# Kernel tuning notes

Hardware: AMD Instinct MI355X
Metric: run time of the kernel (lower is better)

Reference implementation:

```python
import jax, jax.numpy as jnp
import numpy as np

B, N, DIM = 2, 2048, 1024
HEADS, DIM_HEAD = 16, 64
ALIBI_HEADS = 8
NUM_MEM_KV = 4
SCALE = DIM_HEAD ** -0.5


def alibi_slopes(n):
    # standard ALiBi geometric slopes for power-of-2 head counts
    start = 2.0 ** (-8.0 / n)
    return jnp.array([start ** (k + 1) for k in range(n)], dtype=jnp.float32)


def alibi_bias(i, j, heads, total_heads):
    # symmetric ALiBi: bias = -|k_pos - q_pos| * slope; unbiased heads padded with zeros at front
    range_q = jnp.arange(j - i, j)          # query absolute positions (offset by mem kv)
    range_k = jnp.arange(j)
    rel = -jnp.abs(range_k[None, :] - range_q[:, None]).astype(jnp.float32)  # [i, j]
    slopes = alibi_slopes(heads)
    bias = slopes[:, None, None] * rel[None]                                  # [heads, i, j]
    pad = jnp.zeros((total_heads - heads, i, j), dtype=bias.dtype)
    return jnp.concatenate([pad, bias], axis=0)                               # [total_heads, i, j]


def setup_inputs() -> dict:
    key = jax.random.key(0)
    ks = jax.random.split(key, 7)
    w = lambda k, s: jax.random.normal(k, s, jnp.float32) * 0.02
    return {
        "x": jax.random.normal(ks[0], (B, N, DIM), jnp.float32),
        "mask": jnp.ones((B, N), dtype=bool),
        "Wq": w(ks[1], (DIM, HEADS * DIM_HEAD)),
        "Wk": w(ks[2], (DIM, HEADS * DIM_HEAD)),
        "Wv": w(ks[3], (DIM, HEADS * DIM_HEAD)),
        "Wo": w(ks[4], (HEADS * DIM_HEAD, DIM)),
        "mem_k": jax.random.normal(ks[5], (HEADS, NUM_MEM_KV, DIM_HEAD), jnp.float32),
        "mem_v": jax.random.normal(ks[6], (HEADS, NUM_MEM_KV, DIM_HEAD), jnp.float32),
    }


def reference(x, mask, Wq, Wk, Wv, Wo, mem_k, mem_v):
    b, n, _ = x.shape
    h, d, m = HEADS, DIM_HEAD, NUM_MEM_KV
    # QKV projections (Linear, no bias)
    q = (x @ Wq).reshape(b, n, h, d).transpose(0, 2, 1, 3)  # [b,h,n,d]
    k = (x @ Wk).reshape(b, n, h, d).transpose(0, 2, 1, 3)
    v = (x @ Wv).reshape(b, n, h, d).transpose(0, 2, 1, 3)
    # prepend learned memory key/values
    k = jnp.concatenate([jnp.broadcast_to(mem_k[None], (b, h, m, d)), k], axis=2)
    v = jnp.concatenate([jnp.broadcast_to(mem_v[None], (b, h, m, d)), v], axis=2)
    i, j = n, n + m
    # input mask padded with True over memory positions
    input_mask = jnp.concatenate([jnp.ones((b, m), dtype=bool), mask], axis=1)  # [b,j]
    # causal mask: key kj attendable by query qi iff kj - (j - i) <= qi (mem keys always visible)
    qpos = jnp.arange(i)[:, None]
    kpos = jnp.arange(j)[None, :]
    causal_allow = (kpos - (j - i)) <= qpos                                      # [i,j]
    allow = input_mask[:, None, None, :] & causal_allow[None, None]              # [b,1,i,j]
    bias = alibi_bias(i, j, ALIBI_HEADS, h)                                      # [h,i,j]
    scores = jnp.einsum('bhid,bhjd->bhij', q, k) * SCALE + bias[None]
    scores = jnp.where(allow, scores, jnp.finfo(scores.dtype).min)
    attn = jax.nn.softmax(scores, axis=-1)
    out = jnp.einsum('bhij,bhjd->bhid', attn, v)
    out = out.transpose(0, 2, 1, 3).reshape(b, n, h * d) @ Wo
    return out * mask[..., None].astype(out.dtype)
```

## Files before the change

kernel.cpp:

```cpp
#include <hip/hip_runtime.h>

typedef __bf16 bf16x8 __attribute__((ext_vector_type(8)));
typedef float f32x4 __attribute__((ext_vector_type(4)));
typedef unsigned short us8 __attribute__((ext_vector_type(8)));
typedef unsigned short ushort_t;
typedef unsigned int uint_t;

constexpr int BATCH = 2;
constexpr int SEQ   = 2048;
constexpr int DIM   = 1024;
constexpr int HEADS = 16;
constexpr int DH    = 64;
constexpr int NKV   = 4;
constexpr int KROWS = 2080;
constexpr int KVSTR = 133120;
constexpr float QSCALE = 0.18033688011112042f;

__device__ inline ushort_t f2bf(float f) {
  uint_t u = __builtin_bit_cast(uint_t, f);
  u += 0x7FFFu + ((u >> 16) & 1u);
  return (ushort_t)(u >> 16);
}

__device__ inline uint_t cvtpk(float a, float b) {
  uint_t r;
  asm("v_cvt_pk_bf16_f32 %0, %1, %2" : "=v"(r) : "v"(a), "v"(b));
  return r;
}

__device__ inline float ex2(float x) { return __builtin_amdgcn_exp2f(x); }

__device__ inline bf16x8 mk8(uint_t a, uint_t b, uint_t c, uint_t d) {
  union { uint_t u[4]; bf16x8 v; } x;
  x.u[0] = a; x.u[1] = b; x.u[2] = c; x.u[3] = d;
  return x.v;
}

__device__ inline size_t swz(int row, int k) {
  return ((size_t)(row >> 7) << 17) +
         (size_t)(((k >> 3) << 7) + (row & 127)) * 8 + (k & 7);
}

__device__ inline int koff(int j, int d) {
  return ((j >> 4) << 10) + ((d >> 3) << 7) + ((j & 15) << 3) + (d & 7);
}
__device__ inline int voff(int j, int d) {
  int w = j & 31;
  int kap = ((w & 12) << 1) | (w & 3) | ((w >> 4) << 2);
  return ((j >> 5) << 11) + ((kap >> 3) << 9) + (d << 3) + (kap & 7);
}

__device__ inline void g2l16(const ushort_t* g, ushort_t* l) {
  __builtin_amdgcn_global_load_lds(
      (const __attribute__((address_space(1))) void*)g,
      (__attribute__((address_space(3))) void*)l, 16, 0, 0);
}

__global__ __launch_bounds__(256) void prep_kernel(
    const float* __restrict__ x,
    const float* __restrict__ W0, const float* __restrict__ W1,
    const float* __restrict__ W2, const float* __restrict__ W3,
    const float* __restrict__ memk, const float* __restrict__ memv,
    ushort_t* __restrict__ xb,
    ushort_t* __restrict__ T0, ushort_t* __restrict__ T1,
    ushort_t* __restrict__ T2, ushort_t* __restrict__ T3,
    ushort_t* __restrict__ Vt, ushort_t* __restrict__ Ka)
{
  __shared__ float tile[32][33];
  int bid = blockIdx.x, t = threadIdx.x;
  if (bid < 2048) {
    int idx = bid * 256 + t;
    const float4* s = (const float4*)x;
    float4 a = s[idx * 2], bq = s[idx * 2 + 1];
    us8 o;
    o[0] = f2bf(a.x);  o[1] = f2bf(a.y);  o[2] = f2bf(a.z);  o[3] = f2bf(a.w);
    o[4] = f2bf(bq.x); o[5] = f2bf(bq.y); o[6] = f2bf(bq.z); o[7] = f2bf(bq.w);
    int e = idx * 8, row = e >> 10, k = e & 1023;
    *(us8*)&xb[swz(row, k)] = o;
  } else if (bid < 6144) {
    int tb = bid - 2048, z = tb >> 10, r2 = tb & 1023;
    int bx = r2 & 31, by = r2 >> 5;
    const float* W = (z == 0) ? W0 : (z == 1) ? W1 : (z == 2) ? W2 : W3;
    ushort_t* T = (z == 0) ? T0 : (z == 1) ? T1 : (z == 2) ? T2 : T3;
    float sc = (z == 0) ? QSCALE : 1.0f;
    int tx = t & 31, ty = t >> 5;
    int kb = bx * 32, nb = by * 32;
    for (int y = ty; y < 32; y += 8)
      tile[y][tx] = W[(size_t)(kb + y) * 1024 + nb + tx];
    __syncthreads();
    for (int y = ty; y < 32; y += 8)
      T[swz(nb + y, kb + tx)] = f2bf(tile[tx][y] * sc);
  } else {
    int idx = (bid - 6144) * 256 + t;
    if (idx < 8192) {
      int j = idx & 3, d = (idx >> 2) & 63, h = (idx >> 8) & 15, b = idx >> 12;
      Vt[(size_t)(b * 16 + h) * KVSTR + voff(j, d)] =
          f2bf(memv[((size_t)h * NKV + j) * DH + d]);
    } else if (idx < 16384) {
      int k2 = idx - 8192;
      int d = k2 & 63, j = (k2 >> 6) & 3, h = (k2 >> 8) & 15, b = k2 >> 12;
      Ka[(size_t)(b * 16 + h) * KVSTR + koff(j, d)] =
          f2bf(memk[((size_t)h * NKV + j) * DH + d]);
    }
  }
}

__global__ __launch_bounds__(256, 6) void gemm_bt(
    const ushort_t* __restrict__ A,
    const ushort_t* __restrict__ Wt0, const ushort_t* __restrict__ Wt1,
    const ushort_t* __restrict__ Wt2,
    ushort_t* __restrict__ C0, ushort_t* __restrict__ Ka,
    ushort_t* __restrict__ Vt)
{
  __shared__ ushort_t As[8192];
  __shared__ ushort_t Bs[4096];
  int bid = blockIdx.x;
  int xcd = bid & 7, g = bid >> 3;
  int z = g >> 6, rem = g & 63;
  int my = (xcd >> 1) * 8 + (rem >> 3);
  int nx = (xcd & 1) * 8 + (rem & 7);
  const ushort_t* Wt = (z == 1) ? Wt1 : (z == 2) ? Wt2 : Wt0;
  int t = threadIdx.x;
  int lane = t & 63, wave = t >> 6;
  int col = lane & 15, quad = lane >> 4;
  int m0 = my * 128, n0 = nx * 64;
  int moff = wave * 32;
  int nhalf = nx & 1;

  const ushort_t* Abase = A  + ((size_t)(m0 >> 7) << 17);
  const ushort_t* Bbase = Wt + ((size_t)(nx >> 1) << 17);
  int so = wave * 2048 + lane * 8;

  f32x4 acc[2][4] = {};

  for (int k0 = 0; k0 < DIM; k0 += 64) {
    __syncthreads();
    const ushort_t* Ak = Abase + ((size_t)k0 << 7);
    const ushort_t* Bk = Bbase + ((size_t)k0 << 7);
#pragma unroll
    for (int c2 = 0; c2 < 4; c2++)
      g2l16(Ak + so + c2 * 512, &As[so + c2 * 512]);
#pragma unroll
    for (int c2 = 0; c2 < 2; c2++) {
      int ko = wave * 2 + c2;
      g2l16(Bk + ko * 1024 + nhalf * 512 + lane * 8, &Bs[ko * 512 + lane * 8]);
    }
    __syncthreads();
#pragma unroll
    for (int kc = 0; kc < 2; kc++) {
      bf16x8 af[2], bfr[4];
#pragma unroll
      for (int mi = 0; mi < 2; mi++)
        af[mi] = *(const bf16x8*)&As[(kc * 4 + quad) * 1024 + (moff + mi * 16 + col) * 8];
#pragma unroll
      for (int ni = 0; ni < 4; ni++)
        bfr[ni] = *(const bf16x8*)&Bs[(kc * 4 + quad) * 512 + (ni * 16 + col) * 8];
#pragma unroll
      for (int mi = 0; mi < 2; mi++)
#pragma unroll
        for (int ni = 0; ni < 4; ni++)
          acc[mi][ni] = __builtin_amdgcn_mfma_f32_16x16x32_bf16(
              af[mi], bfr[ni], acc[mi][ni], 0, 0, 0);
    }
  }

  if (z == 0) {
#pragma unroll
    for (int mi = 0; mi < 2; mi++) {
      int row0 = m0 + moff + mi * 16 + quad * 4;
#pragma unroll
      for (int ni = 0; ni < 4; ni++) {
        int cn = n0 + ni * 16 + col;
#pragma unroll
        for (int r = 0; r < 4; r++)
          C0[swz(row0 + r, cn)] = f2bf(acc[mi][ni][r]);
      }
    }
  } else if (z == 1) {
#pragma unroll
    for (int mi = 0; mi < 2; mi++) {
      int gi = m0 + moff + mi * 16 + quad * 4;
      int bq = gi >> 11, i = gi & 2047;
#pragma unroll
      for (int ni = 0; ni < 4; ni++) {
        int feat = n0 + ni * 16 + col;
        int hh = feat >> 6, dd = feat & 63;
        size_t base = (size_t)(bq * 16 + hh) * KVSTR;
#pragma unroll
        for (int r = 0; r < 4; r++)
          Ka[base + koff(i + r + NKV, dd)] = f2bf(acc[mi][ni][r]);
      }
    }
  } else {
#pragma unroll
    for (int mi = 0; mi < 2; mi++) {
      int gi = m0 + moff + mi * 16 + quad * 4;
      int bq = gi >> 11, i = gi & 2047;
#pragma unroll
      for (int ni = 0; ni < 4; ni++) {
        int feat = n0 + ni * 16 + col;
        int hh = feat >> 6, dd = feat & 63;
        size_t vb = (size_t)(bq * 16 + hh) * KVSTR;
#pragma unroll
        for (int r = 0; r < 4; r++)
          Vt[vb + voff(i + r + NKV, dd)] = f2bf(acc[mi][ni][r]);
      }
    }
  }
}

__global__ __launch_bounds__(256, 4) void gemm_out64(
    const ushort_t* __restrict__ A, const ushort_t* __restrict__ Wt,
    float* __restrict__ Cf)
{
  __shared__ ushort_t As[4096];
  __shared__ ushort_t Bs[4096];
  int bid = blockIdx.x;
  int xcd = bid & 7, g = bid >> 3;
  int my = xcd * 8 + (g >> 4);
  int nx = g & 15;
  int t = threadIdx.x;
  int lane = t & 63, wave = t >> 6;
  int col = lane & 15, quad = lane >> 4;
  int m0 = my * 64, n0 = nx * 64;
  int mhalf = my & 1;
  int nhalf = nx & 1;

  const ushort_t* Abase = A  + ((size_t)(my >> 1) << 17);
  const ushort_t* Bbase = Wt + ((size_t)(nx >> 1) << 17);

  f32x4 acc[4] = {};

  for (int k0 = 0; k0 < DIM; k0 += 64) {
    __syncthreads();
    const ushort_t* Ak = Abase + ((size_t)k0 << 7);
    const ushort_t* Bk = Bbase + ((size_t)k0 << 7);
#pragma unroll
    for (int c2 = 0; c2 < 2; c2++) {
      int ko = wave * 2 + c2;
      g2l16(Ak + ko * 1024 + mhalf * 512 + lane * 8, &As[ko * 512 + lane * 8]);
      g2l16(Bk + ko * 1024 + nhalf * 512 + lane * 8, &Bs[ko * 512 + lane * 8]);
    }
    __syncthreads();
#pragma unroll
    for (int kc = 0; kc < 2; kc++) {
      bf16x8 af, bfr[4];
      af = *(const bf16x8*)&As[(kc * 4 + quad) * 512 + (wave * 16 + col) * 8];
#pragma unroll
      for (int ni = 0; ni < 4; ni++)
        bfr[ni] = *(const bf16x8*)&Bs[(kc * 4 + quad) * 512 + (ni * 16 + col) * 8];
#pragma unroll
      for (int ni = 0; ni < 4; ni++)
        acc[ni] = __builtin_amdgcn_mfma_f32_16x16x32_bf16(
            af, bfr[ni], acc[ni], 0, 0, 0);
    }
  }

  int row0 = m0 + wave * 16 + quad * 4;
#pragma unroll
  for (int ni = 0; ni < 4; ni++) {
    int cn = n0 + ni * 16 + col;
#pragma unroll
    for (int r = 0; r < 4; r++)
      Cf[(size_t)(row0 + r) * DIM + cn] = acc[ni][r];
  }
}

#define STRIPC(jbX, I0, Q00, Q01, Q10, Q11,                                   \
               O0A, O1A, O2A, O3A, OLA, O0B, O1B, O2B, O3B, OLB,              \
               K0, K1, K2, K3, V0, V1, V2, V3)                                \
  {                                                                           \
    f32x4 s0a = {}, s1a = {}, s0b = {}, s1b = {};                             \
    __builtin_amdgcn_s_setprio(1);                                            \
    s0a = __builtin_amdgcn_mfma_f32_16x16x32_bf16(K0, Q00, s0a, 0, 0, 0);     \
    s0a = __builtin_amdgcn_mfma_f32_16x16x32_bf16(K1, Q01, s0a, 0, 0, 0);     \
    s1a = __builtin_amdgcn_mfma_f32_16x16x32_bf16(K2, Q00, s1a, 0, 0, 0);     \
    s1a = __builtin_amdgcn_mfma_f32_16x16x32_bf16(K3, Q01, s1a, 0, 0, 0);     \
    s0b = __builtin_amdgcn_mfma_f32_16x16x32_bf16(K0, Q10, s0b, 0, 0, 0);     \
    s0b = __builtin_amdgcn_mfma_f32_16x16x32_bf16(K1, Q11, s0b, 0, 0, 0);     \
    s1b = __builtin_amdgcn_mfma_f32_16x16x32_bf16(K2, Q10, s1b, 0, 0, 0);     \
    s1b = __builtin_amdgcn_mfma_f32_16x16x32_bf16(K3, Q11, s1b, 0, 0, 0);     \
    __builtin_amdgcn_s_setprio(0);                                            \
    float fD0 = (float)((jbX) + quad * 4 - (I0) - col - NKV);                 \
    bf16x8 pa, pb;                                                            \
    {                                                                         \
      f32x4 e0, e1;                                                           \
      if ((jbX) <= (I0) - 27) {                                               \
        _Pragma("unroll")                                                     \
        for (int r = 0; r < 4; r++) {                                         \
          e0[r] = ex2(fmaf(slope2, fD0 + (float)r, s0a[r]));                  \
          e1[r] = ex2(fmaf(slope2, fD0 + 16.0f + (float)r, s1a[r]));          \
        }                                                                     \
      } else {                                                                \
        _Pragma("unroll")                                                     \
        for (int r = 0; r < 4; r++) {                                         \
          float f0 = fD0 + (float)r, f1 = fD0 + 16.0f + (float)r;             \
          float w0 = fmaf(slope2, f0, s0a[r]);                                \
          float w1 = fmaf(slope2, f1, s1a[r]);                                \
          w0 = (f0 <= 0.0f) ? w0 : -1e30f;                                    \
          w1 = (f1 <= 0.0f) ? w1 : -1e30f;                                    \
          e0[r] = ex2(w0); e1[r] = ex2(w1);                                   \
        }                                                                     \
      }                                                                       \
      pa = mk8(cvtpk(e0[0], e0[1]), cvtpk(e0[2], e0[3]),                      \
               cvtpk(e1[0], e1[1]), cvtpk(e1[2], e1[3]));                     \
    }                                                                         \
    {                                                                         \
      float fDb = fD0 - 16.0f;                                                \
      f32x4 e0, e1;                                                           \
      if ((jbX) <= (I0) - 11) {                                               \
        _Pragma("unroll")                                                     \
        for (int r = 0; r < 4; r++) {                                         \
          e0[r] = ex2(fmaf(slope2, fDb + (float)r, s0b[r]));                  \
          e1[r] = ex2(fmaf(slope2, fDb + 16.0f + (float)r, s1b[r]));          \
        }                                                                     \
      } else {                                                                \
        _Pragma("unroll")                                                     \
        for (int r = 0; r < 4; r++) {                                         \
          float f0 = fDb + (float)r, f1 = fDb + 16.0f + (float)r;             \
          float w0 = fmaf(slope2, f0, s0b[r]);                                \
          float w1 = fmaf(slope2, f1, s1b[r]);                                \
          w0 = (f0 <= 0.0f) ? w0 : -1e30f;                                    \
          w1 = (f1 <= 0.0f) ? w1 : -1e30f;                                    \
          e0[r] = ex2(w0); e1[r] = ex2(w1);                                   \
        }                                                                     \
      }                                                                       \
      pb = mk8(cvtpk(e0[0], e0[1]), cvtpk(e0[2], e0[3]),                      \
               cvtpk(e1[0], e1[1]), cvtpk(e1[2], e1[3]));                     \
    }                                                                         \
    __builtin_amdgcn_s_setprio(1);                                            \
    O0A = __builtin_amdgcn_mfma_f32_16x16x32_bf16(pa, V0, O0A, 0, 0, 0);      \
    O1A = __builtin_amdgcn_mfma_f32_16x16x32_bf16(pa, V1, O1A, 0, 0, 0);      \
    O2A = __builtin_amdgcn_mfma_f32_16x16x32_bf16(pa, V2, O2A, 0, 0, 0);      \
    O3A = __builtin_amdgcn_mfma_f32_16x16x32_bf16(pa, V3, O3A, 0, 0, 0);      \
    OLA = __builtin_amdgcn_mfma_f32_16x16x32_bf16(pa, ones, OLA, 0, 0, 0);    \
    O0B = __builtin_amdgcn_mfma_f32_16x16x32_bf16(pb, V0, O0B, 0, 0, 0);      \
    O1B = __builtin_amdgcn_mfma_f32_16x16x32_bf16(pb, V1, O1B, 0, 0, 0);      \
    O2B = __builtin_amdgcn_mfma_f32_16x16x32_bf16(pb, V2, O2B, 0, 0, 0);      \
    O3B = __builtin_amdgcn_mfma_f32_16x16x32_bf16(pb, V3, O3B, 0, 0, 0);      \
    OLB = __builtin_amdgcn_mfma_f32_16x16x32_bf16(pb, ones, OLB, 0, 0, 0);    \
    __builtin_amdgcn_s_setprio(0);                                            \
  }

#define SUBITER(jbX, jpref, K0, K1, K2, K3, V0, V1, V2, V3)                   \
  {                                                                           \
    STRIPC(jbX, i0y, qy00, qy01, qy10, qy11,                                  \
           yo0a, yo1a, yo2a, yo3a, yla, yo0b, yo1b, yo2b, yo3b, ylb,          \
           K0, K1, K2, K3, V0, V1, V2, V3);                                   \
    if ((jbX) < jendx) {                                                      \
      STRIPC(jbX, i0x, qx00, qx01, qx10, qx11,                                \
             xo0a, xo1a, xo2a, xo3a, xla, xo0b, xo1b, xo2b, xo3b, xlb,        \
             K0, K1, K2, K3, V0, V1, V2, V3);                                 \
    }                                                                         \
    int jc = (jpref) > 2048 ? 2048 : (jpref);                                 \
    int aK = jc * 64 + kOff;                                                  \
    K0 = *(const bf16x8*)&Kbh[aK];                                            \
    K1 = *(const bf16x8*)&Kbh[aK + 512];                                      \
    K2 = *(const bf16x8*)&Kbh[aK + 1024];                                     \
    K3 = *(const bf16x8*)&Kbh[aK + 1536];                                     \
    int aV = jc * 64 + vOff;                                                  \
    V0 = *(const bf16x8*)&Vbh[aV];                                            \
    V1 = *(const bf16x8*)&Vbh[aV + 128];                                      \
    V2 = *(const bf16x8*)&Vbh[aV + 256];                                      \
    V3 = *(const bf16x8*)&Vbh[aV + 384];                                      \
  }

__global__ __launch_bounds__(256) void attn_kernel(
    const ushort_t* __restrict__ Q, const ushort_t* __restrict__ Ka,
    const ushort_t* __restrict__ Vt, ushort_t* __restrict__ AO)
{
  __shared__ __align__(16) float Cmb[2][10][64][4];
  int t = threadIdx.x, lane = t & 63, wave = t >> 6;
  int col = lane & 15, quad = lane >> 4;
  int bid = blockIdx.x;
  int xcd = bid & 7, slot = bid >> 3;
  int bh = xcd + 8 * (slot >> 4);
  int b = bh >> 4, h = bh & 15;
  int u = slot & 15;
  int pi = u * 2 + (wave >> 1);
  int h2 = wave & 1;
  int p2 = wave >> 1;
  float slope2 = (h < 8) ? 0.0f : exp2f(-(float)(h - 7)) * 1.4426950408889634f;

  const ushort_t* Kbh = Ka + (size_t)bh * KVSTR;
  const ushort_t* Vbh = Vt + (size_t)bh * KVSTR;

  us8 ones_u = {0x3F80, 0x3F80, 0x3F80, 0x3F80, 0x3F80, 0x3F80, 0x3F80, 0x3F80};
  bf16x8 ones = __builtin_bit_cast(bf16x8, ones_u);

  int kOff = quad * 128 + col * 8;
  int vOff = quad * 512 + col * 8;

  int i0x = pi * 32;
  int i0y = 2016 - pi * 32;
  int jendx = ((i0x + 67) >> 5) << 5;
  int jendy = ((i0y + 67) >> 5) << 5;

  bf16x8 qx00 = *(const bf16x8*)&Q[swz(b * SEQ + i0x + col, h * DH + quad * 8)];
  bf16x8 qx01 = *(const bf16x8*)&Q[swz(b * SEQ + i0x + col, h * DH + 32 + quad * 8)];
  bf16x8 qx10 = *(const bf16x8*)&Q[swz(b * SEQ + i0x + 16 + col, h * DH + quad * 8)];
  bf16x8 qx11 = *(const bf16x8*)&Q[swz(b * SEQ + i0x + 16 + col, h * DH + 32 + quad * 8)];
  bf16x8 qy00 = *(const bf16x8*)&Q[swz(b * SEQ + i0y + col, h * DH + quad * 8)];
  bf16x8 qy01 = *(const bf16x8*)&Q[swz(b * SEQ + i0y + col, h * DH + 32 + quad * 8)];
  bf16x8 qy10 = *(const bf16x8*)&Q[swz(b * SEQ + i0y + 16 + col, h * DH + quad * 8)];
  bf16x8 qy11 = *(const bf16x8*)&Q[swz(b * SEQ + i0y + 16 + col, h * DH + 32 + quad * 8)];

  f32x4 xo0a = {}, xo1a = {}, xo2a = {}, xo3a = {}, xla = {};
  f32x4 xo0b = {}, xo1b = {}, xo2b = {}, xo3b = {}, xlb = {};
  f32x4 yo0a = {}, yo1a = {}, yo2a = {}, yo3a = {}, yla = {};
  f32x4 yo0b = {}, yo1b = {}, yo2b = {}, yo3b = {}, ylb = {};

  bf16x8 ka0, ka1, ka2, ka3, va0, va1, va2, va3;
  bf16x8 kb0, kb1, kb2, kb3, vb0, vb1, vb2, vb3;
  int jb0 = h2 * 32;
  {
    int aK = jb0 * 64 + kOff, aV = jb0 * 64 + vOff;
    ka0 = *(const bf16x8*)&Kbh[aK];
    ka1 = *(const bf16x8*)&Kbh[aK + 512];
    ka2 = *(const bf16x8*)&Kbh[aK + 1024];
    ka3 = *(const bf16x8*)&Kbh[aK + 1536];
    va0 = *(const bf16x8*)&Vbh[aV];
    va1 = *(const bf16x8*)&Vbh[aV + 128];
    va2 = *(const bf16x8*)&Vbh[aV + 256];
    va3 = *(const bf16x8*)&Vbh[aV + 384];
    int j1 = jb0 + 64;
    int bK = j1 * 64 + kOff, bV = j1 * 64 + vOff;
    kb0 = *(const bf16x8*)&Kbh[bK];
    kb1 = *(const bf16x8*)&Kbh[bK + 512];
    kb2 = *(const bf16x8*)&Kbh[bK + 1024];
    kb3 = *(const bf16x8*)&Kbh[bK + 1536];
    vb0 = *(const bf16x8*)&Vbh[bV];
    vb1 = *(const bf16x8*)&Vbh[bV + 128];
    vb2 = *(const bf16x8*)&Vbh[bV + 256];
    vb3 = *(const bf16x8*)&Vbh[bV + 384];
  }

  int ntrip = (jendy - jb0 + 127) >> 7;
  int jb = jb0;
#pragma unroll 1
  for (int tr = 0; tr < ntrip; tr++, jb += 128) {
    SUBITER(jb, jb + 128, ka0, ka1, ka2, ka3, va0, va1, va2, va3);
    SUBITER(jb + 64, jb + 192, kb0, kb1, kb2, kb3, vb0, vb1, vb2, vb3);
  }

  if (h2 == 1) {
    *(f32x4*)&Cmb[p2][0][lane][0] = yo0a;
    *(f32x4*)&Cmb[p2][1][lane][0] = yo1a;
    *(f32x4*)&Cmb[p2][2][lane][0] = yo2a;
    *(f32x4*)&Cmb[p2][3][lane][0] = yo3a;
    *(f32x4*)&Cmb[p2][4][lane][0] = yla;
    *(f32x4*)&Cmb[p2][5][lane][0] = yo0b;
    *(f32x4*)&Cmb[p2][6][lane][0] = yo1b;
    *(f32x4*)&Cmb[p2][7][lane][0] = yo2b;
    *(f32x4*)&Cmb[p2][8][lane][0] = yo3b;
    *(f32x4*)&Cmb[p2][9][lane][0] = ylb;
  }
  __syncthreads();
  if (h2 == 0) {
    yo0a += *(const f32x4*)&Cmb[p2][0][lane][0];
    yo1a += *(const f32x4*)&Cmb[p2][1][lane][0];
    yo2a += *(const f32x4*)&Cmb[p2][2][lane][0];
    yo3a += *(const f32x4*)&Cmb[p2][3][lane][0];
    yla  += *(const f32x4*)&Cmb[p2][4][lane][0];
    yo0b += *(const f32x4*)&Cmb[p2][5][lane][0];
    yo1b += *(const f32x4*)&Cmb[p2][6][lane][0];
    yo2b += *(const f32x4*)&Cmb[p2][7][lane][0];
    yo3b += *(const f32x4*)&Cmb[p2][8][lane][0];
    ylb  += *(const f32x4*)&Cmb[p2][9][lane][0];
#pragma unroll
    for (int r = 0; r < 4; r++) {
      float linv = __builtin_amdgcn_rcpf(yla[r]);
      int row = b * SEQ + i0y + quad * 4 + r;
      AO[swz(row, h * DH + col)]      = f2bf(yo0a[r] * linv);
      AO[swz(row, h * DH + 16 + col)] = f2bf(yo1a[r] * linv);
      AO[swz(row, h * DH + 32 + col)] = f2bf(yo2a[r] * linv);
      AO[swz(row, h * DH + 48 + col)] = f2bf(yo3a[r] * linv);
    }
#pragma unroll
    for (int r = 0; r < 4; r++) {
      float linv = __builtin_amdgcn_rcpf(ylb[r]);
      int row = b * SEQ + i0y + 16 + quad * 4 + r;
      AO[swz(row, h * DH + col)]      = f2bf(yo0b[r] * linv);
      AO[swz(row, h * DH + 16 + col)] = f2bf(yo1b[r] * linv);
      AO[swz(row, h * DH + 32 + col)] = f2bf(yo2b[r] * linv);
      AO[swz(row, h * DH + 48 + col)] = f2bf(yo3b[r] * linv);
    }
  }
  __syncthreads();

  if (h2 == 1) {
    *(f32x4*)&Cmb[p2][0][lane][0] = xo0a;
    *(f32x4*)&Cmb[p2][1][lane][0] = xo1a;
    *(f32x4*)&Cmb[p2][2][lane][0] = xo2a;
    *(f32x4*)&Cmb[p2][3][lane][0] = xo3a;
    *(f32x4*)&Cmb[p2][4][lane][0] = xla;
    *(f32x4*)&Cmb[p2][5][lane][0] = xo0b;
    *(f32x4*)&Cmb[p2][6][lane][0] = xo1b;
    *(f32x4*)&Cmb[p2][7][lane][0] = xo2b;
    *(f32x4*)&Cmb[p2][8][lane][0] = xo3b;
    *(f32x4*)&Cmb[p2][9][lane][0] = xlb;
  }
  __syncthreads();
  if (h2 == 0) {
    xo0a += *(const f32x4*)&Cmb[p2][0][lane][0];
    xo1a += *(const f32x4*)&Cmb[p2][1][lane][0];
    xo2a += *(const f32x4*)&Cmb[p2][2][lane][0];
    xo3a += *(const f32x4*)&Cmb[p2][3][lane][0];
    xla  += *(const f32x4*)&Cmb[p2][4][lane][0];
    xo0b += *(const f32x4*)&Cmb[p2][5][lane][0];
    xo1b += *(const f32x4*)&Cmb[p2][6][lane][0];
    xo2b += *(const f32x4*)&Cmb[p2][7][lane][0];
    xo3b += *(const f32x4*)&Cmb[p2][8][lane][0];
    xlb  += *(const f32x4*)&Cmb[p2][9][lane][0];
#pragma unroll
    for (int r = 0; r < 4; r++) {
      float linv = __builtin_amdgcn_rcpf(xla[r]);
      int row = b * SEQ + i0x + quad * 4 + r;
      AO[swz(row, h * DH + col)]      = f2bf(xo0a[r] * linv);
      AO[swz(row, h * DH + 16 + col)] = f2bf(xo1a[r] * linv);
      AO[swz(row, h * DH + 32 + col)] = f2bf(xo2a[r] * linv);
      AO[swz(row, h * DH + 48 + col)] = f2bf(xo3a[r] * linv);
    }
#pragma unroll
    for (int r = 0; r < 4; r++) {
      float linv = __builtin_amdgcn_rcpf(xlb[r]);
      int row = b * SEQ + i0x + 16 + quad * 4 + r;
      AO[swz(row, h * DH + col)]      = f2bf(xo0b[r] * linv);
      AO[swz(row, h * DH + 16 + col)] = f2bf(xo1b[r] * linv);
      AO[swz(row, h * DH + 32 + col)] = f2bf(xo2b[r] * linv);
      AO[swz(row, h * DH + 48 + col)] = f2bf(xo3b[r] * linv);
    }
  }
}
#undef SUBITER
#undef STRIPC

extern "C" void kernel_launch(void* const* d_in, const int* in_sizes, int n_in,
                              void* d_out, int out_size, void* d_ws, size_t ws_size,
                              hipStream_t stream)
{
  const float* x    = (const float*)d_in[0];
  const float* Wq   = (const float*)d_in[2];
  const float* Wk   = (const float*)d_in[3];
  const float* Wv   = (const float*)d_in[4];
  const float* Wo   = (const float*)d_in[5];
  const float* memk = (const float*)d_in[6];
  const float* memv = (const float*)d_in[7];
  float* out = (float*)d_out;

  char* ws = (char*)d_ws;
  size_t off = 0;
  auto alloc = [&](size_t bytes) {
    char* p = ws + off;
    off += (bytes + 255) & ~(size_t)255;
    return p;
  };
  ushort_t* WqT = (ushort_t*)alloc((size_t)1024 * 1024 * 2);
  ushort_t* WkT = (ushort_t*)alloc((size_t)1024 * 1024 * 2);
  ushort_t* WvT = (ushort_t*)alloc((size_t)1024 * 1024 * 2);
  ushort_t* WoT = (ushort_t*)alloc((size_t)1024 * 1024 * 2);
  ushort_t* xb  = (ushort_t*)alloc((size_t)4096 * 1024 * 2);
  ushort_t* Qb  = (ushort_t*)alloc((size_t)4096 * 1024 * 2);
  ushort_t* Ka  = (ushort_t*)alloc((size_t)32 * KVSTR * 2);
  ushort_t* Vt  = (ushort_t*)alloc((size_t)32 * KVSTR * 2);
  ushort_t* AO  = xb;

  prep_kernel<<<dim3(6208), dim3(256), 0, stream>>>(
      x, Wq, Wk, Wv, Wo, memk, memv, xb, WqT, WkT, WvT, WoT, Vt, Ka);
  gemm_bt<<<dim3(1536), dim3(256), 0, stream>>>(xb, WqT, WkT, WvT, Qb, Ka, Vt);
  attn_kernel<<<dim3(512), dim3(256), 0, stream>>>(Qb, Ka, Vt, AO);
  gemm_out64<<<dim3(1024), dim3(256), 0, stream>>>(AO, WoT, out);
}
```

Before: 188.5 us.

## Fuse QKV GEMM blocks to share A tiles; split attention keys across four waves

The QKV projection now uses one 512-thread block per output tile. Each block computes Q, K and V together, so each loaded x tile is reused for three weight tiles instead of being fetched by three separate blocks. The attention kernel now has each block process two query-strip pairs in sequence, with all four waves splitting the key range in stride-256 chunks, and the partial results of three waves are merged by wave 0. This cuts redundant activation loads and changes how work is balanced across waves. In exchange it adds more LDS traffic and barriers per strip, and gives the GEMM fewer, larger blocks.

```diff
diff --git a/kernel.cpp b/kernel.cpp
--- a/kernel.cpp
+++ b/kernel.cpp
@@ -105,7 +105,7 @@
   }
 }
 
-__global__ __launch_bounds__(256, 6) void gemm_bt(
+__global__ __launch_bounds__(512) void gemm_bt(
     const ushort_t* __restrict__ A,
     const ushort_t* __restrict__ Wt0, const ushort_t* __restrict__ Wt1,
     const ushort_t* __restrict__ Wt2,
@@ -113,98 +113,87 @@
     ushort_t* __restrict__ Vt)
 {
   __shared__ ushort_t As[8192];
-  __shared__ ushort_t Bs[4096];
+  __shared__ ushort_t Bs[12288];
   int bid = blockIdx.x;
   int xcd = bid & 7, g = bid >> 3;
-  int z = g >> 6, rem = g & 63;
-  int my = (xcd >> 1) * 8 + (rem >> 3);
-  int nx = (xcd & 1) * 8 + (rem & 7);
-  const ushort_t* Wt = (z == 1) ? Wt1 : (z == 2) ? Wt2 : Wt0;
+  int my = (xcd >> 1) * 8 + (g >> 3);
+  int nx = (xcd & 1) * 8 + (g & 7);
   int t = threadIdx.x;
   int lane = t & 63, wave = t >> 6;
   int col = lane & 15, quad = lane >> 4;
   int m0 = my * 128, n0 = nx * 64;
-  int moff = wave * 32;
+  int moff = wave * 16;
   int nhalf = nx & 1;
 
-  const ushort_t* Abase = A  + ((size_t)(m0 >> 7) << 17);
-  const ushort_t* Bbase = Wt + ((size_t)(nx >> 1) << 17);
-  int so = wave * 2048 + lane * 8;
-
-  f32x4 acc[2][4] = {};
+  const ushort_t* Abase = A + ((size_t)(m0 >> 7) << 17);
+  size_t boff = (size_t)(nx >> 1) << 17;
+  const ushort_t* Bb0 = Wt0 + boff;
+  const ushort_t* Bb1 = Wt1 + boff;
+  const ushort_t* Bb2 = Wt2 + boff;
+  int t8 = t * 8;
+  int bo = (t >> 6) * 1024 + nhalf * 512 + (t & 63) * 8;
+
+  f32x4 acc[3][4] = {};
 
   for (int k0 = 0; k0 < DIM; k0 += 64) {
     __syncthreads();
     const ushort_t* Ak = Abase + ((size_t)k0 << 7);
-    const ushort_t* Bk = Bbase + ((size_t)k0 << 7);
-#pragma unroll
-    for (int c2 = 0; c2 < 4; c2++)
-      g2l16(Ak + so + c2 * 512, &As[so + c2 * 512]);
-#pragma unroll
-    for (int c2 = 0; c2 < 2; c2++) {
-      int ko = wave * 2 + c2;
-      g2l16(Bk + ko * 1024 + nhalf * 512 + lane * 8, &Bs[ko * 512 + lane * 8]);
-    }
+    size_t ko2 = (size_t)k0 << 7;
+    g2l16(Ak + t8, &As[t8]);
+    g2l16(Ak + t8 + 4096, &As[t8 + 4096]);
+    g2l16(Bb0 + ko2 + bo, &Bs[t8]);
+    g2l16(Bb1 + ko2 + bo, &Bs[4096 + t8]);
+    g2l16(Bb2 + ko2 + bo, &Bs[8192 + t8]);
     __syncthreads();
 #pragma unroll
     for (int kc = 0; kc < 2; kc++) {
-      bf16x8 af[2], bfr[4];
-#pragma unroll
-      for (int mi = 0; mi < 2; mi++)
-        af[mi] = *(const bf16x8*)&As[(kc * 4 + quad) * 1024 + (moff + mi * 16 + col) * 8];
-#pragma unroll
-      for (int ni = 0; ni < 4; ni++)
-        bfr[ni] = *(const bf16x8*)&Bs[(kc * 4 + quad) * 512 + (ni * 16 + col) * 8];
-#pragma unroll
-      for (int mi = 0; mi < 2; mi++)
+      bf16x8 af = *(const bf16x8*)&As[(kc * 4 + quad) * 1024 + (moff + col) * 8];
+#pragma unroll
+      for (int z = 0; z < 3; z++) {
+        bf16x8 bfr[4];
 #pragma unroll
         for (int ni = 0; ni < 4; ni++)
-          acc[mi][ni] = __builtin_amdgcn_mfma_f32_16x16x32_bf16(
-              af[mi], bfr[ni], acc[mi][ni], 0, 0, 0);
-    }
-  }
-
-  if (z == 0) {
-#pragma unroll
-    for (int mi = 0; mi < 2; mi++) {
-      int row0 = m0 + moff + mi * 16 + quad * 4;
-#pragma unroll
-      for (int ni = 0; ni < 4; ni++) {
-        int cn = n0 + ni * 16 + col;
-#pragma unroll
-        for (int r = 0; r < 4; r++)
-          C0[swz(row0 + r, cn)] = f2bf(acc[mi][ni][r]);
-      }
-    }
-  } else if (z == 1) {
-#pragma unroll
-    for (int mi = 0; mi < 2; mi++) {
-      int gi = m0 + moff + mi * 16 + quad * 4;
-      int bq = gi >> 11, i = gi & 2047;
-#pragma unroll
-      for (int ni = 0; ni < 4; ni++) {
-        int feat = n0 + ni * 16 + col;
-        int hh = feat >> 6, dd = feat & 63;
-        size_t base = (size_t)(bq * 16 + hh) * KVSTR;
-#pragma unroll
-        for (int r = 0; r < 4; r++)
-          Ka[base + koff(i + r + NKV, dd)] = f2bf(acc[mi][ni][r]);
-      }
-    }
-  } else {
-#pragma unroll
-    for (int mi = 0; mi < 2; mi++) {
-      int gi = m0 + moff + mi * 16 + quad * 4;
-      int bq = gi >> 11, i = gi & 2047;
-#pragma unroll
-      for (int ni = 0; ni < 4; ni++) {
-        int feat = n0 + ni * 16 + col;
-        int hh = feat >> 6, dd = feat & 63;
-        size_t vb = (size_t)(bq * 16 + hh) * KVSTR;
-#pragma unroll
-        for (int r = 0; r < 4; r++)
-          Vt[vb + voff(i + r + NKV, dd)] = f2bf(acc[mi][ni][r]);
-      }
+          bfr[ni] = *(const bf16x8*)&Bs[z * 4096 + (kc * 4 + quad) * 512 + (ni * 16 + col) * 8];
+#pragma unroll
+        for (int ni = 0; ni < 4; ni++)
+          acc[z][ni] = __builtin_amdgcn_mfma_f32_16x16x32_bf16(
+              af, bfr[ni], acc[z][ni], 0, 0, 0);
+      }
+    }
+  }
+
+  int row0 = m0 + moff + quad * 4;
+  {
+#pragma unroll
+    for (int ni = 0; ni < 4; ni++) {
+      int cn = n0 + ni * 16 + col;
+#pragma unroll
+      for (int r = 0; r < 4; r++)
+        C0[swz(row0 + r, cn)] = f2bf(acc[0][ni][r]);
+    }
+  }
+  {
+    int bq = row0 >> 11, i = row0 & 2047;
+#pragma unroll
+    for (int ni = 0; ni < 4; ni++) {
+      int feat = n0 + ni * 16 + col;
+      int hh = feat >> 6, dd = feat & 63;
+      size_t base = (size_t)(bq * 16 + hh) * KVSTR;
+#pragma unroll
+      for (int r = 0; r < 4; r++)
+        Ka[base + koff(i + r + NKV, dd)] = f2bf(acc[1][ni][r]);
+    }
+  }
+  {
+    int bq = row0 >> 11, i = row0 & 2047;
+#pragma unroll
+    for (int ni = 0; ni < 4; ni++) {
+      int feat = n0 + ni * 16 + col;
+      int hh = feat >> 6, dd = feat & 63;
+      size_t vb = (size_t)(bq * 16 + hh) * KVSTR;
+#pragma unroll
+      for (int r = 0; r < 4; r++)
+        Vt[vb + voff(i + r + NKV, dd)] = f2bf(acc[2][ni][r]);
     }
   }
 }
@@ -369,17 +358,14 @@
     const ushort_t* __restrict__ Q, const ushort_t* __restrict__ Ka,
     const ushort_t* __restrict__ Vt, ushort_t* __restrict__ AO)
 {
-  __shared__ __align__(16) float Cmb[2][10][64][4];
+  __shared__ __align__(16) float Cmb[3][10][64][4];
   int t = threadIdx.x, lane = t & 63, wave = t >> 6;
   int col = lane & 15, quad = lane >> 4;
   int bid = blockIdx.x;
   int xcd = bid & 7, slot = bid >> 3;
   int bh = xcd + 8 * (slot >> 4);
   int b = bh >> 4, h = bh & 15;
-  int u = slot & 15;
-  int pi = u * 2 + (wave >> 1);
-  int h2 = wave & 1;
-  int p2 = wave >> 1;
+  int q = slot & 15;
   float slope2 = (h < 8) ? 0.0f : exp2f(-(float)(h - 7)) * 1.4426950408889634f;
 
   const ushort_t* Kbh = Ka + (size_t)bh * KVSTR;
@@ -391,145 +377,157 @@
   int kOff = quad * 128 + col * 8;
   int vOff = quad * 512 + col * 8;
 
-  int i0x = pi * 32;
-  int i0y = 2016 - pi * 32;
-  int jendx = ((i0x + 67) >> 5) << 5;
-  int jendy = ((i0y + 67) >> 5) << 5;
-
-  bf16x8 qx00 = *(const bf16x8*)&Q[swz(b * SEQ + i0x + col, h * DH + quad * 8)];
-  bf16x8 qx01 = *(const bf16x8*)&Q[swz(b * SEQ + i0x + col, h * DH + 32 + quad * 8)];
-  bf16x8 qx10 = *(const bf16x8*)&Q[swz(b * SEQ + i0x + 16 + col, h * DH + quad * 8)];
-  bf16x8 qx11 = *(const bf16x8*)&Q[swz(b * SEQ + i0x + 16 + col, h * DH + 32 + quad * 8)];
-  bf16x8 qy00 = *(const bf16x8*)&Q[swz(b * SEQ + i0y + col, h * DH + quad * 8)];
-  bf16x8 qy01 = *(const bf16x8*)&Q[swz(b * SEQ + i0y + col, h * DH + 32 + quad * 8)];
-  bf16x8 qy10 = *(const bf16x8*)&Q[swz(b * SEQ + i0y + 16 + col, h * DH + quad * 8)];
-  bf16x8 qy11 = *(const bf16x8*)&Q[swz(b * SEQ + i0y + 16 + col, h * DH + 32 + quad * 8)];
-
-  f32x4 xo0a = {}, xo1a = {}, xo2a = {}, xo3a = {}, xla = {};
-  f32x4 xo0b = {}, xo1b = {}, xo2b = {}, xo3b = {}, xlb = {};
-  f32x4 yo0a = {}, yo1a = {}, yo2a = {}, yo3a = {}, yla = {};
-  f32x4 yo0b = {}, yo1b = {}, yo2b = {}, yo3b = {}, ylb = {};
-
-  bf16x8 ka0, ka1, ka2, ka3, va0, va1, va2, va3;
-  bf16x8 kb0, kb1, kb2, kb3, vb0, vb1, vb2, vb3;
-  int jb0 = h2 * 32;
-  {
-    int aK = jb0 * 64 + kOff, aV = jb0 * 64 + vOff;
-    ka0 = *(const bf16x8*)&Kbh[aK];
-    ka1 = *(const bf16x8*)&Kbh[aK + 512];
-    ka2 = *(const bf16x8*)&Kbh[aK + 1024];
-    ka3 = *(const bf16x8*)&Kbh[aK + 1536];
-    va0 = *(const bf16x8*)&Vbh[aV];
-    va1 = *(const bf16x8*)&Vbh[aV + 128];
-    va2 = *(const bf16x8*)&Vbh[aV + 256];
-    va3 = *(const bf16x8*)&Vbh[aV + 384];
-    int j1 = jb0 + 64;
-    int bK = j1 * 64 + kOff, bV = j1 * 64 + vOff;
-    kb0 = *(const bf16x8*)&Kbh[bK];
-    kb1 = *(const bf16x8*)&Kbh[bK + 512];
-    kb2 = *(const bf16x8*)&Kbh[bK + 1024];
-    kb3 = *(const bf16x8*)&Kbh[bK + 1536];
-    vb0 = *(const bf16x8*)&Vbh[bV];
-    vb1 = *(const bf16x8*)&Vbh[bV + 128];
-    vb2 = *(const bf16x8*)&Vbh[bV + 256];
-    vb3 = *(const bf16x8*)&Vbh[bV + 384];
-  }
-
-  int ntrip = (jendy - jb0 + 127) >> 7;
-  int jb = jb0;
+  for (int pr = 0; pr < 2; pr++) {
+    int m = pr ? (31 - q) : q;
+    int i0x = m * 32;
+    int i0y = 2016 - m * 32;
+    int jendx = ((i0x + 67) >> 5) << 5;
+    int jendy = ((i0y + 67) >> 5) << 5;
+
+    bf16x8 qx00 = *(const bf16x8*)&Q[swz(b * SEQ + i0x + col, h * DH + quad * 8)];
+    bf16x8 qx01 = *(const bf16x8*)&Q[swz(b * SEQ + i0x + col, h * DH + 32 + quad * 8)];
+    bf16x8 qx10 = *(const bf16x8*)&Q[swz(b * SEQ + i0x + 16 + col, h * DH + quad * 8)];
+    bf16x8 qx11 = *(const bf16x8*)&Q[swz(b * SEQ + i0x + 16 + col, h * DH + 32 + quad * 8)];
+    bf16x8 qy00 = *(const bf16x8*)&Q[swz(b * SEQ + i0y + col, h * DH + quad * 8)];
+    bf16x8 qy01 = *(const bf16x8*)&Q[swz(b * SEQ + i0y + col, h * DH + 32 + quad * 8)];
+    bf16x8 qy10 = *(const bf16x8*)&Q[swz(b * SEQ + i0y + 16 + col, h * DH + quad * 8)];
+    bf16x8 qy11 = *(const bf16x8*)&Q[swz(b * SEQ + i0y + 16 + col, h * DH + 32 + quad * 8)];
+
+    f32x4 xo0a = {}, xo1a = {}, xo2a = {}, xo3a = {}, xla = {};
+    f32x4 xo0b = {}, xo1b = {}, xo2b = {}, xo3b = {}, xlb = {};
+    f32x4 yo0a = {}, yo1a = {}, yo2a = {}, yo3a = {}, yla = {};
+    f32x4 yo0b = {}, yo1b = {}, yo2b = {}, yo3b = {}, ylb = {};
+
+    bf16x8 ka0, ka1, ka2, ka3, va0, va1, va2, va3;
+    bf16x8 kb0, kb1, kb2, kb3, vb0, vb1, vb2, vb3;
+    int jb0 = wave * 32;
+    {
+      int aK = jb0 * 64 + kOff, aV = jb0 * 64 + vOff;
+      ka0 = *(const bf16x8*)&Kbh[aK];
+      ka1 = *(const bf16x8*)&Kbh[aK + 512];
+      ka2 = *(const bf16x8*)&Kbh[aK + 1024];
+      ka3 = *(const bf16x8*)&Kbh[aK + 1536];
+      va0 = *(const bf16x8*)&Vbh[aV];
+      va1 = *(const bf16x8*)&Vbh[aV + 128];
+      va2 = *(const bf16x8*)&Vbh[aV + 256];
+      va3 = *(const bf16x8*)&Vbh[aV + 384];
+      int j1 = jb0 + 128;
+      int bK = j1 * 64 + kOff, bV = j1 * 64 + vOff;
+      kb0 = *(const bf16x8*)&Kbh[bK];
+      kb1 = *(const bf16x8*)&Kbh[bK + 512];
+      kb2 = *(const bf16x8*)&Kbh[bK + 1024];
+      kb3 = *(const bf16x8*)&Kbh[bK + 1536];
+      vb0 = *(const bf16x8*)&Vbh[bV];
+      vb1 = *(const bf16x8*)&Vbh[bV + 128];
+      vb2 = *(const bf16x8*)&Vbh[bV + 256];
+      vb3 = *(const bf16x8*)&Vbh[bV + 384];
+    }
+
+    int ntrip = (jendy - jb0 + 255) >> 8;
+    int jb = jb0;
 #pragma unroll 1
-  for (int tr = 0; tr < ntrip; tr++, jb += 128) {
-    SUBITER(jb, jb + 128, ka0, ka1, ka2, ka3, va0, va1, va2, va3);
-    SUBITER(jb + 64, jb + 192, kb0, kb1, kb2, kb3, vb0, vb1, vb2, vb3);
-  }
-
-  if (h2 == 1) {
-    *(f32x4*)&Cmb[p2][0][lane][0] = yo0a;
-    *(f32x4*)&Cmb[p2][1][lane][0] = yo1a;
-    *(f32x4*)&Cmb[p2][2][lane][0] = yo2a;
-    *(f32x4*)&Cmb[p2][3][lane][0] = yo3a;
-    *(f32x4*)&Cmb[p2][4][lane][0] = yla;
-    *(f32x4*)&Cmb[p2][5][lane][0] = yo0b;
-    *(f32x4*)&Cmb[p2][6][lane][0] = yo1b;
-    *(f32x4*)&Cmb[p2][7][lane][0] = yo2b;
-    *(f32x4*)&Cmb[p2][8][lane][0] = yo3b;
-    *(f32x4*)&Cmb[p2][9][lane][0] = ylb;
-  }
-  __syncthreads();
-  if (h2 == 0) {
-    yo0a += *(const f32x4*)&Cmb[p2][0][lane][0];
-    yo1a += *(const f32x4*)&Cmb[p2][1][lane][0];
-    yo2a += *(const f32x4*)&Cmb[p2][2][lane][0];
-    yo3a += *(const f32x4*)&Cmb[p2][3][lane][0];
-    yla  += *(const f32x4*)&Cmb[p2][4][lane][0];
-    yo0b += *(const f32x4*)&Cmb[p2][5][lane][0];
-    yo1b += *(const f32x4*)&Cmb[p2][6][lane][0];
-    yo2b += *(const f32x4*)&Cmb[p2][7][lane][0];
-    yo3b += *(const f32x4*)&Cmb[p2][8][lane][0];
-    ylb  += *(const f32x4*)&Cmb[p2][9][lane][0];
-#pragma unroll
-    for (int r = 0; r < 4; r++) {
-      float linv = __builtin_amdgcn_rcpf(yla[r]);
-      int row = b * SEQ + i0y + quad * 4 + r;
-      AO[swz(row, h * DH + col)]      = f2bf(yo0a[r] * linv);
-      AO[swz(row, h * DH + 16 + col)] = f2bf(yo1a[r] * linv);
-      AO[swz(row, h * DH + 32 + col)] = f2bf(yo2a[r] * linv);
-      AO[swz(row, h * DH + 48 + col)] = f2bf(yo3a[r] * linv);
-    }
-#pragma unroll
-    for (int r = 0; r < 4; r++) {
-      float linv = __builtin_amdgcn_rcpf(ylb[r]);
-      int row = b * SEQ + i0y + 16 + quad * 4 + r;
-      AO[swz(row, h * DH + col)]      = f2bf(yo0b[r] * linv);
-      AO[swz(row, h * DH + 16 + col)] = f2bf(yo1b[r] * linv);
-      AO[swz(row, h * DH + 32 + col)] = f2bf(yo2b[r] * linv);
-      AO[swz(row, h * DH + 48 + col)] = f2bf(yo3b[r] * linv);
-    }
-  }
-  __syncthreads();
-
-  if (h2 == 1) {
-    *(f32x4*)&Cmb[p2][0][lane][0] = xo0a;
-    *(f32x4*)&Cmb[p2][1][lane][0] = xo1a;
-    *(f32x4*)&Cmb[p2][2][lane][0] = xo2a;
-    *(f32x4*)&Cmb[p2][3][lane][0] = xo3a;
-    *(f32x4*)&Cmb[p2][4][lane][0] = xla;
-    *(f32x4*)&Cmb[p2][5][lane][0] = xo0b;
-    *(f32x4*)&Cmb[p2][6][lane][0] = xo1b;
-    *(f32x4*)&Cmb[p2][7][lane][0] = xo2b;
-    *(f32x4*)&Cmb[p2][8][lane][0] = xo3b;
-    *(f32x4*)&Cmb[p2][9][lane][0] = xlb;
-  }
-  __syncthreads();
-  if (h2 == 0) {
-    xo0a += *(const f32x4*)&Cmb[p2][0][lane][0];
-    xo1a += *(const f32x4*)&Cmb[p2][1][lane][0];
-    xo2a += *(const f32x4*)&Cmb[p2][2][lane][0];
-    xo3a += *(const f32x4*)&Cmb[p2][3][lane][0];
-    xla  += *(const f32x4*)&Cmb[p2][4][lane][0];
-    xo0b += *(const f32x4*)&Cmb[p2][5][lane][0];
-    xo1b += *(const f32x4*)&Cmb[p2][6][lane][0];
-    xo2b += *(const f32x4*)&Cmb[p2][7][lane][0];
-    xo3b += *(const f32x4*)&Cmb[p2][8][lane][0];
-    xlb  += *(const f32x4*)&Cmb[p2][9][lane][0];
-#pragma unroll
-    for (int r = 0; r < 4; r++) {
-      float linv = __builtin_amdgcn_rcpf(xla[r]);
-      int row = b * SEQ + i0x + quad * 4 + r;
-      AO[swz(row, h * DH + col)]      = f2bf(xo0a[r] * linv);
-      AO[swz(row, h * DH + 16 + col)] = f2bf(xo1a[r] * linv);
-      AO[swz(row, h * DH + 32 + col)] = f2bf(xo2a[r] * linv);
-      AO[swz(row, h * DH + 48 + col)] = f2bf(xo3a[r] * linv);
-    }
-#pragma unroll
-    for (int r = 0; r < 4; r++) {
-      float linv = __builtin_amdgcn_rcpf(xlb[r]);
-      int row = b * SEQ + i0x + 16 + quad * 4 + r;
-      AO[swz(row, h * DH + col)]      = f2bf(xo0b[r] * linv);
-      AO[swz(row, h * DH + 16 + col)] = f2bf(xo1b[r] * linv);
-      AO[swz(row, h * DH + 32 + col)] = f2bf(xo2b[r] * linv);
-      AO[swz(row, h * DH + 48 + col)] = f2bf(xo3b[r] * linv);
-    }
+    for (int tr = 0; tr < ntrip; tr++, jb += 256) {
+      SUBITER(jb, jb + 256, ka0, ka1, ka2, ka3, va0, va1, va2, va3);
+      SUBITER(jb + 128, jb + 384, kb0, kb1, kb2, kb3, vb0, vb1, vb2, vb3);
+    }
+
+    if (wave) {
+      int w = wave - 1;
+      *(f32x4*)&Cmb[w][0][lane][0] = yo0a;
+      *(f32x4*)&Cmb[w][1][lane][0] = yo1a;
+      *(f32x4*)&Cmb[w][2][lane][0] = yo2a;
+      *(f32x4*)&Cmb[w][3][lane][0] = yo3a;
+      *(f32x4*)&Cmb[w][4][lane][0] = yla;
+      *(f32x4*)&Cmb[w][5][lane][0] = yo0b;
+      *(f32x4*)&Cmb[w][6][lane][0] = yo1b;
+      *(f32x4*)&Cmb[w][7][lane][0] = yo2b;
+      *(f32x4*)&Cmb[w][8][lane][0] = yo3b;
+      *(f32x4*)&Cmb[w][9][lane][0] = ylb;
+    }
+    __syncthreads();
+    if (wave == 0) {
+#pragma unroll
+      for (int w = 0; w < 3; w++) {
+        yo0a += *(const f32x4*)&Cmb[w][0][lane][0];
+        yo1a += *(const f32x4*)&Cmb[w][1][lane][0];
+        yo2a += *(const f32x4*)&Cmb[w][2][lane][0];
+        yo3a += *(const f32x4*)&Cmb[w][3][lane][0];
+        yla  += *(const f32x4*)&Cmb[w][4][lane][0];
+        yo0b += *(const f32x4*)&Cmb[w][5][lane][0];
+        yo1b += *(const f32x4*)&Cmb[w][6][lane][0];
+        yo2b += *(const f32x4*)&Cmb[w][7][lane][0];
+        yo3b += *(const f32x4*)&Cmb[w][8][lane][0];
+        ylb  += *(const f32x4*)&Cmb[w][9][lane][0];
+      }
+#pragma unroll
+      for (int r = 0; r < 4; r++) {
+        float linv = __builtin_amdgcn_rcpf(yla[r]);
+        int row = b * SEQ + i0y + quad * 4 + r;
+        AO[swz(row, h * DH + col)]      = f2bf(yo0a[r] * linv);
+        AO[swz(row, h * DH + 16 + col)] = f2bf(yo1a[r] * linv);
+        AO[swz(row, h * DH + 32 + col)] = f2bf(yo2a[r] * linv);
+        AO[swz(row, h * DH + 48 + col)] = f2bf(yo3a[r] * linv);
+      }
+#pragma unroll
+      for (int r = 0; r < 4; r++) {
+        float linv = __builtin_amdgcn_rcpf(ylb[r]);
+        int row = b * SEQ + i0y + 16 + quad * 4 + r;
+        AO[swz(row, h * DH + col)]      = f2bf(yo0b[r] * linv);
+        AO[swz(row, h * DH + 16 + col)] = f2bf(yo1b[r] * linv);
+        AO[swz(row, h * DH + 32 + col)] = f2bf(yo2b[r] * linv);
+        AO[swz(row, h * DH + 48 + col)] = f2bf(yo3b[r] * linv);
+      }
+    }
+    __syncthreads();
+
+    if (wave) {
+      int w = wave - 1;
+      *(f32x4*)&Cmb[w][0][lane][0] = xo0a;
+      *(f32x4*)&Cmb[w][1][lane][0] = xo1a;
+      *(f32x4*)&Cmb[w][2][lane][0] = xo2a;
+      *(f32x4*)&Cmb[w][3][lane][0] = xo3a;
+      *(f32x4*)&Cmb[w][4][lane][0] = xla;
+      *(f32x4*)&Cmb[w][5][lane][0] = xo0b;
+      *(f32x4*)&Cmb[w][6][lane][0] = xo1b;
+      *(f32x4*)&Cmb[w][7][lane][0] = xo2b;
+      *(f32x4*)&Cmb[w][8][lane][0] = xo3b;
+      *(f32x4*)&Cmb[w][9][lane][0] = xlb;
+    }
+    __syncthreads();
+    if (wave == 0) {
+#pragma unroll
+      for (int w = 0; w < 3; w++) {
+        xo0a += *(const f32x4*)&Cmb[w][0][lane][0];
+        xo1a += *(const f32x4*)&Cmb[w][1][lane][0];
+        xo2a += *(const f32x4*)&Cmb[w][2][lane][0];
+        xo3a += *(const f32x4*)&Cmb[w][3][lane][0];
+        xla  += *(const f32x4*)&Cmb[w][4][lane][0];
+        xo0b += *(const f32x4*)&Cmb[w][5][lane][0];
+        xo1b += *(const f32x4*)&Cmb[w][6][lane][0];
+        xo2b += *(const f32x4*)&Cmb[w][7][lane][0];
+        xo3b += *(const f32x4*)&Cmb[w][8][lane][0];
+        xlb  += *(const f32x4*)&Cmb[w][9][lane][0];
+      }
+#pragma unroll
+      for (int r = 0; r < 4; r++) {
+        float linv = __builtin_amdgcn_rcpf(xla[r]);
+        int row = b * SEQ + i0x + quad * 4 + r;
+        AO[swz(row, h * DH + col)]      = f2bf(xo0a[r] * linv);
+        AO[swz(row, h * DH + 16 + col)] = f2bf(xo1a[r] * linv);
+        AO[swz(row, h * DH + 32 + col)] = f2bf(xo2a[r] * linv);
+        AO[swz(row, h * DH + 48 + col)] = f2bf(xo3a[r] * linv);
+      }
+#pragma unroll
+      for (int r = 0; r < 4; r++) {
+        float linv = __builtin_amdgcn_rcpf(xlb[r]);
+        int row = b * SEQ + i0x + 16 + quad * 4 + r;
+        AO[swz(row, h * DH + col)]      = f2bf(xo0b[r] * linv);
+        AO[swz(row, h * DH + 16 + col)] = f2bf(xo1b[r] * linv);
+        AO[swz(row, h * DH + 32 + col)] = f2bf(xo2b[r] * linv);
+        AO[swz(row, h * DH + 48 + col)] = f2bf(xo3b[r] * linv);
+      }
+    }
+    __syncthreads();
   }
 }
 #undef SUBITER
@@ -567,7 +565,7 @@
 
   prep_kernel<<<dim3(6208), dim3(256), 0, stream>>>(
       x, Wq, Wk, Wv, Wo, memk, memv, xb, WqT, WkT, WvT, WoT, Vt, Ka);
-  gemm_bt<<<dim3(1536), dim3(256), 0, stream>>>(xb, WqT, WkT, WvT, Qb, Ka, Vt);
+  gemm_bt<<<dim3(512), dim3(512), 0, stream>>>(xb, WqT, WkT, WvT, Qb, Ka, Vt);
   attn_kernel<<<dim3(512), dim3(256), 0, stream>>>(Qb, Ka, Vt, AO);
   gemm_out64<<<dim3(1024), dim3(256), 0, stream>>>(AO, WoT, out);
 }
```

Measured after the change: 192.6 us. +2.2%, slower.
